# Optimization experiments

Hardware: AMD Instinct MI355X
Metric: run time of the kernel (lower is better)

Reference implementation:

```python
import jax, jax.numpy as jnp
import numpy as np

# BERT-base geometry
B, N, H, DH = 4, 512, 12, 64
HID = H * DH            # 768
E = 65536               # total edges (~avg degree 32)
NREL = 64               # relation vocabulary


def setup_inputs() -> dict:
    key = jax.random.key(0)
    ks = jax.random.split(key, 12)
    node_states = jax.random.normal(ks[0], (B, N, HID), jnp.float32)
    b = jax.random.randint(ks[1], (E,), 0, B)
    hn = jax.random.randint(ks[2], (E,), 0, N)
    tn = jax.random.randint(ks[3], (E,), 0, N)
    r = jax.random.randint(ks[4], (E,), 0, NREL)
    edge_indices = jnp.stack([b, hn, tn, r]).astype(jnp.int32)  # (4, E)
    node_type_ids = jnp.zeros((B, N), jnp.int32)  # unused by this subclass
    sc = 0.02
    Wq = jax.random.normal(ks[5], (HID, HID), jnp.float32) * sc
    bq = jnp.zeros((HID,), jnp.float32)
    Wk = jax.random.normal(ks[6], (HID, HID), jnp.float32) * sc
    bk = jnp.zeros((HID,), jnp.float32)
    Wv = jax.random.normal(ks[7], (HID, HID), jnp.float32) * sc
    bv = jnp.zeros((HID,), jnp.float32)
    # relation matrix embeddings: one (DH, DH) matrix per relation id
    rel_emb = jnp.eye(DH, dtype=jnp.float32)[None] + jax.random.normal(ks[8], (NREL, DH, DH), jnp.float32) * sc
    return {"node_states": node_states, "edge_indices": edge_indices,
            "node_type_ids": node_type_ids, "Wq": Wq, "bq": bq,
            "Wk": Wk, "bk": bk, "Wv": Wv, "bv": bv, "rel_emb": rel_emb}


def reference(node_states, edge_indices, node_type_ids, Wq, bq, Wk, bk, Wv, bv, rel_emb):
    Bq, Nn, hid = node_states.shape
    # dense QKV projections (torch Linear: y = x @ W^T + b)
    Q = node_states @ Wq.T + bq
    K = node_states @ Wk.T + bk
    V = (node_states @ Wv.T + bv).reshape(Bq, Nn, H, DH)  # (B,N,H,D)
    be, he, te, re = edge_indices  # each (E,)
    # per-edge gathers
    Qe = Q[be, he].reshape(-1, H, DH)   # (E,H,D)
    Ke = K[be, te].reshape(-1, H, DH)   # (E,H,D)
    Re = rel_emb[re]                     # (E,D,D) relation matrix per edge
    # Q projected through relation matrix, then inner product with K per head
    Qp = jnp.einsum('ehd,edk->ehk', Qe, Re)
    logits = jnp.einsum('ehd,ehd->eh', Qp, Ke) / jnp.sqrt(jnp.float32(DH))  # (E,H)
    # sparse softmax over tail nodes: segment = (batch, head_node)
    seg = be * Nn + he
    nseg = Bq * Nn
    m = jax.ops.segment_max(logits, seg, num_segments=nseg)      # (BN,H)
    ex = jnp.exp(logits - m[seg])
    denom = jax.ops.segment_sum(ex, seg, num_segments=nseg)      # (BN,H)
    p = ex / denom[seg]                                          # (E,H)
    # dropout prob = 0.0 (deterministic reference)
    # aggregate: out[b,i,h,:] = sum_edges p_e * V[b, tail_e, h, :]
    contrib = p[:, :, None] * V[be, te]                          # (E,H,D)
    out = jax.ops.segment_sum(contrib, seg, num_segments=nseg)   # (BN,H,D)
    return out.reshape(Bq, Nn, H * DH)
```

## Files before the change

kernel.cpp:

```cpp
#include <hip/hip_runtime.h>
#include <hip/hip_bf16.h>

#define NB   4
#define NN   512
#define NH   12
#define DHD  64
#define HID  768
#define NE   65536
#define NSEG 2048
#define NREL 64
#define NSUB 32
#define NRSUB (NREL * NSUB)

typedef short bf16x8 __attribute__((ext_vector_type(8)));
typedef float f32x4  __attribute__((ext_vector_type(4)));

__device__ __forceinline__ unsigned short f2bf(float f) {
    __hip_bfloat16 h = __float2bfloat16(f);
    return *reinterpret_cast<unsigned short*>(&h);
}
__device__ __forceinline__ float bf2f(unsigned short s) {
    return __int_as_float(((int)s) << 16);
}
__device__ __forceinline__ void load_lds16(const void* g, void* l) {
    __builtin_amdgcn_global_load_lds(
        (const __attribute__((address_space(1))) unsigned int*)g,
        (__attribute__((address_space(3))) unsigned int*)l, 16, 0, 0);
}

#define NX4 ((2048 * 768) / 4)
#define NW4 ((768 * 768) / 4)
__global__ __launch_bounds__(256) void cast_kernel(
    const float* __restrict__ X, const float* __restrict__ Wq,
    const float* __restrict__ Wk, const float* __restrict__ Wv,
    unsigned short* __restrict__ Xh, unsigned short* __restrict__ Wh)
{
    const int i = blockIdx.x * 256 + threadIdx.x;
    float4 v;
    ushort4* dst;
    if (i < NX4) {
        v = ((const float4*)X)[i];
        dst = &((ushort4*)Xh)[i];
    } else {
        const int j = i - NX4;
        const float* W = (j < NW4) ? Wq : ((j < 2 * NW4) ? Wk : Wv);
        const int jj = (j < NW4) ? j : ((j < 2 * NW4) ? j - NW4 : j - 2 * NW4);
        v = ((const float4*)W)[jj];
        dst = &((ushort4*)Wh)[j];
    }
    ushort4 r;
    r.x = f2bf(v.x); r.y = f2bf(v.y); r.z = f2bf(v.z); r.w = f2bf(v.w);
    *dst = r;
}

__global__ __launch_bounds__(256) void qkv_mfma(
    const unsigned short* __restrict__ Xh, const unsigned short* __restrict__ Wh,
    const float* __restrict__ bq, const float* __restrict__ bk,
    const float* __restrict__ bv,
    unsigned short* __restrict__ Qh, unsigned short* __restrict__ Kh,
    float* __restrict__ Vo)
{
    const int z = blockIdx.z;
    const unsigned short* W = Wh + (size_t)z * (768 * 768);
    const float* bias = (z == 0) ? bq : ((z == 1) ? bk : bv);

    const int n0 = blockIdx.x * 128;
    const int m0 = blockIdx.y * 128;
    const int tid  = threadIdx.x;
    const int lane = tid & 63;
    const int wave = tid >> 6;
    const int wm = wave >> 1, wn = wave & 1;

    __shared__ unsigned short As[128 * 64];
    __shared__ unsigned short Bs[128 * 64];

    f32x4 acc[4][4];
    #pragma unroll
    for (int a = 0; a < 4; ++a)
        #pragma unroll
        for (int b = 0; b < 4; ++b) acc[a][b] = (f32x4){0.f, 0.f, 0.f, 0.f};

    const int ml = lane & 15;
    const int q4 = lane >> 4;

    for (int k0 = 0; k0 < HID; k0 += 64) {
        __syncthreads();
        #pragma unroll
        for (int l = 0; l < 4; ++l) {
            const int idx = (l * 4 + wave) * 64 + lane;
            const int row = idx >> 3;
            const int kq  = (idx & 7) ^ (row & 7);
            load_lds16(Xh + (size_t)(m0 + row) * HID + k0 + kq * 8,
                       As + (l * 4 + wave) * 512);
            load_lds16(W + (size_t)(n0 + row) * HID + k0 + kq * 8,
                       Bs + (l * 4 + wave) * 512);
        }
        __syncthreads();

        #pragma unroll
        for (int ks = 0; ks < 2; ++ks) {
            bf16x8 af[4], bfr[4];
            #pragma unroll
            for (int t = 0; t < 4; ++t) {
                const int ar = wm * 64 + t * 16 + ml;
                const int ac = (ks * 4 + q4) ^ (ar & 7);
                af[t] = *(const bf16x8*)(As + ar * 64 + ac * 8);
                const int br = wn * 64 + t * 16 + ml;
                const int bc = (ks * 4 + q4) ^ (br & 7);
                bfr[t] = *(const bf16x8*)(Bs + br * 64 + bc * 8);
            }
            #pragma unroll
            for (int mt = 0; mt < 4; ++mt)
                #pragma unroll
                for (int nt = 0; nt < 4; ++nt)
                    acc[mt][nt] = __builtin_amdgcn_mfma_f32_16x16x32_bf16(
                        af[mt], bfr[nt], acc[mt][nt], 0, 0, 0);
        }
    }

    #pragma unroll
    for (int nt = 0; nt < 4; ++nt) {
        const int col = n0 + wn * 64 + nt * 16 + ml;
        const float bcol = bias[col];
        #pragma unroll
        for (int mt = 0; mt < 4; ++mt) {
            const int row = m0 + wm * 64 + mt * 16 + q4 * 4;
            #pragma unroll
            for (int rg = 0; rg < 4; ++rg) {
                const float v = acc[mt][nt][rg] + bcol;
                const size_t o = (size_t)(row + rg) * HID + col;
                if (z == 0)      Qh[o] = f2bf(v);
                else if (z == 1) Kh[o] = f2bf(v);
                else             Vo[o] = v;
            }
        }
    }
}

__global__ void hist_kernel(const int* __restrict__ ei,
                            int* __restrict__ count, int* __restrict__ rcount2)
{
    const int e = blockIdx.x * 256 + threadIdx.x;
    const int b  = ei[e];
    const int hn = ei[NE + e];
    const int rr = ei[3 * NE + e];
    const int sub = (e >> 8) & (NSUB - 1);
    atomicAdd(&count[b * NN + hn], 1);
    atomicAdd(&rcount2[rr * NSUB + sub], 1);
}

__global__ void scan_kernel(const int* __restrict__ cnt, int* __restrict__ ofs)
{
    __shared__ int buf[256];
    const int tid = threadIdx.x;
    int local[8];
    int s = 0;
    #pragma unroll
    for (int i = 0; i < 8; ++i) { local[i] = cnt[tid * 8 + i]; s += local[i]; }
    buf[tid] = s;
    __syncthreads();
    for (int off = 1; off < 256; off <<= 1) {
        const int v = (tid >= off) ? buf[tid - off] : 0;
        __syncthreads();
        buf[tid] += v;
        __syncthreads();
    }
    int run = buf[tid] - s;
    #pragma unroll
    for (int i = 0; i < 8; ++i) { ofs[tid * 8 + i] = run; run += local[i]; }
    if (tid == 255) ofs[2048] = run;
}

__global__ void scatter_kernel(const int* __restrict__ ei, const int* __restrict__ offs,
                               int* __restrict__ cursor,
                               const int* __restrict__ rofs2, int* __restrict__ rcursor2,
                               int* __restrict__ s_te, int* __restrict__ s_seg,
                               int* __restrict__ r_pos)
{
    const int e = blockIdx.x * 256 + threadIdx.x;
    const int b  = ei[e];
    const int hn = ei[NE + e];
    const int tn = ei[2 * NE + e];
    const int rr = ei[3 * NE + e];
    const int sub = (e >> 8) & (NSUB - 1);
    const int seg = b * NN + hn;
    const int pos = offs[seg] + atomicAdd(&cursor[seg], 1);
    s_te[pos]  = tn;
    s_seg[pos] = seg;
    const int rb = rr * NSUB + sub;
    const int rj = atomicAdd(&rcursor2[rb], 1);
    r_pos[rofs2[rb] + rj] = pos;
}

__global__ __launch_bounds__(256) void rel_logits(
    const unsigned short* __restrict__ Qh, const unsigned short* __restrict__ Kh,
    const float* __restrict__ rel,
    const int* __restrict__ rofs2, const int* __restrict__ r_pos,
    const int* __restrict__ s_te, const int* __restrict__ s_seg,
    float* __restrict__ Lg)
{
    const int r = blockIdx.x;
    const int rstart = rofs2[r * NSUB];
    const int rows = (rofs2[(r + 1) * NSUB] - rstart) * NH;
    const int tid = threadIdx.x;
    const int lane = tid & 63;
    const int wave = tid >> 6;

    __shared__ float ReS[64][65];
    __shared__ int qb[256], kb[256], oi[256];
    __shared__ float QpS[4][16][67];

    {
        const float* Rg = rel + (size_t)r * 4096;
        for (int i = tid; i < 1024; i += 256) {
            const float4 v = ((const float4*)Rg)[i];
            const int row = i >> 4, c4 = (i & 15) * 4;
            ReS[row][c4] = v.x; ReS[row][c4 + 1] = v.y;
            ReS[row][c4 + 2] = v.z; ReS[row][c4 + 3] = v.w;
        }
    }
    __syncthreads();

    bf16x8 bfrag[2][4];
    {
        const int q4 = lane >> 4, n = lane & 15;
        #pragma unroll
        for (int ks = 0; ks < 2; ++ks)
            #pragma unroll
            for (int nt = 0; nt < 4; ++nt) {
                bf16x8 f;
                #pragma unroll
                for (int j = 0; j < 8; ++j)
                    f[j] = (short)f2bf(ReS[ks * 32 + q4 * 8 + j][nt * 16 + n]);
                bfrag[ks][nt] = f;
            }
    }

    for (int t0 = blockIdx.y * 256; t0 < rows; t0 += gridDim.y * 256) {
        __syncthreads();
        {
            const int rowid = t0 + tid;
            if (rowid < rows) {
                const int el = rowid / 12;
                const int h  = rowid - el * 12;
                const int pos = r_pos[rstart + el];
                const int seg = s_seg[pos];
                const int te  = s_te[pos];
                const int b   = seg >> 9;
                qb[tid] = seg * HID + h * 64;
                kb[tid] = (b * NN + te) * HID + h * 64;
                oi[tid] = pos * NH + h;
            } else { qb[tid] = 0; kb[tid] = 0; oi[tid] = -1; }
        }
        __syncthreads();

        for (int g = wave; g < 16; g += 4) {
            const int m = lane & 15, q4 = lane >> 4;
            const int qbase = qb[g * 16 + m];
            f32x4 cfr[4] = {{0,0,0,0},{0,0,0,0},{0,0,0,0},{0,0,0,0}};
            #pragma unroll
            for (int ks = 0; ks < 2; ++ks) {
                const bf16x8 afr = *(const bf16x8*)(Qh + qbase + ks * 32 + q4 * 8);
                #pragma unroll
                for (int nt = 0; nt < 4; ++nt)
                    cfr[nt] = __builtin_amdgcn_mfma_f32_16x16x32_bf16(
                        afr, bfrag[ks][nt], cfr[nt], 0, 0, 0);
            }
            #pragma unroll
            for (int nt = 0; nt < 4; ++nt)
                #pragma unroll
                for (int rg = 0; rg < 4; ++rg)
                    QpS[wave][q4 * 4 + rg][nt * 16 + m] = cfr[nt][rg];
            __syncthreads();

            const int rw = lane >> 2, ch = (lane & 3) * 16;
            const int rowid2 = g * 16 + rw;
            const int kbase = kb[rowid2];
            const bf16x8 k0 = *(const bf16x8*)(Kh + kbase + ch);
            const bf16x8 k1 = *(const bf16x8*)(Kh + kbase + ch + 8);
            float s = 0.f;
            #pragma unroll
            for (int i = 0; i < 8; ++i) {
                s = fmaf(QpS[wave][rw][ch + i],     bf2f((unsigned short)k0[i]), s);
                s = fmaf(QpS[wave][rw][ch + 8 + i], bf2f((unsigned short)k1[i]), s);
            }
            s += __shfl_xor(s, 1, 64);
            s += __shfl_xor(s, 2, 64);
            if ((lane & 3) == 0) {
                const int o = oi[rowid2];
                if (o >= 0) Lg[o] = s * 0.125f;
            }
            __syncthreads();
        }
    }
}

__global__ __launch_bounds__(256) void seg_softmax_agg(
    const float* __restrict__ V, const float* __restrict__ Lg,
    const int* __restrict__ offs, const int* __restrict__ s_te,
    float* __restrict__ out)
{
    const int seg  = blockIdx.x;
    const int tid  = threadIdx.x;
    const int start = offs[seg];
    const int cnt   = offs[seg + 1] - start;
    const int browbase = seg & ~(NN - 1);

    __shared__ float lg[64 * NH];
    __shared__ int   te_s[64];
    __shared__ float mh[NH], lh[NH], ah[NH];

    if (tid < NH) { mh[tid] = -1e30f; lh[tid] = 0.f; }

    float acc0 = 0.f, acc1 = 0.f, acc2 = 0.f;
    const int hh = tid >> 6;
    const int dd = tid & 63;

    for (int c0 = 0; c0 < cnt; c0 += 64) {
        const int cc = min(64, cnt - c0);
        __syncthreads();
        if (tid < cc) te_s[tid] = s_te[start + c0 + tid];
        for (int i = tid; i < cc * NH; i += 256)
            lg[i] = Lg[(start + c0) * NH + i];
        __syncthreads();

        if (tid < NH) {
            const int h = tid;
            float mx = mh[h];
            for (int j = 0; j < cc; ++j) mx = fmaxf(mx, lg[j * NH + h]);
            const float alpha = __expf(mh[h] - mx);
            float ssum = 0.f;
            for (int j = 0; j < cc; ++j) {
                const float p = __expf(lg[j * NH + h] - mx);
                lg[j * NH + h] = p;
                ssum += p;
            }
            lh[h] = lh[h] * alpha + ssum;
            mh[h] = mx;
            ah[h] = alpha;
        }
        __syncthreads();

        const float a0 = ah[hh], a1 = ah[4 + hh], a2 = ah[8 + hh];
        acc0 *= a0; acc1 *= a1; acc2 *= a2;
        for (int j = 0; j < cc; ++j) {
            const int row = browbase + te_s[j];
            const float* __restrict__ Vr = V + (size_t)row * HID + dd;
            acc0 = fmaf(lg[j * NH + hh],     Vr[hh * 64],       acc0);
            acc1 = fmaf(lg[j * NH + 4 + hh], Vr[(4 + hh) * 64], acc1);
            acc2 = fmaf(lg[j * NH + 8 + hh], Vr[(8 + hh) * 64], acc2);
        }
    }
    __syncthreads();

    const float l0 = lh[hh], l1 = lh[4 + hh], l2 = lh[8 + hh];
    float* Yo = out + (size_t)seg * HID;
    Yo[tid]       = (l0 > 0.f) ? acc0 / l0 : 0.f;
    Yo[tid + 256] = (l1 > 0.f) ? acc1 / l1 : 0.f;
    Yo[tid + 512] = (l2 > 0.f) ? acc2 / l2 : 0.f;
}

extern "C" void kernel_launch(void* const* d_in, const int* in_sizes, int n_in,
                              void* d_out, int out_size, void* d_ws, size_t ws_size,
                              hipStream_t stream)
{
    const float* X   = (const float*)d_in[0];
    const int*   EI  = (const int*)d_in[1];
    const float* Wq  = (const float*)d_in[3];
    const float* bq  = (const float*)d_in[4];
    const float* Wk  = (const float*)d_in[5];
    const float* bk  = (const float*)d_in[6];
    const float* Wv  = (const float*)d_in[7];
    const float* bv  = (const float*)d_in[8];
    const float* rel = (const float*)d_in[9];
    float* out = (float*)d_out;

    char* p = (char*)d_ws;
    unsigned short* Qh = (unsigned short*)p;  p += (size_t)NSEG * HID * 2;
    unsigned short* Kh = (unsigned short*)p;  p += (size_t)NSEG * HID * 2;
    float* Vb = (float*)p;                    p += (size_t)NSEG * HID * 4;
    unsigned short* Xh = (unsigned short*)p;
    float* Lg = (float*)p;                    p += (size_t)NE * NH * 4;
    unsigned short* Wh = (unsigned short*)p;  p += (size_t)3 * 768 * 768 * 2;
    int* offs     = (int*)p;                  p += 2052 * 4;
    int* rofs2    = (int*)p;                  p += (NRSUB + 4) * 4;
    int* count    = (int*)p;                  p += NSEG * 4;
    int* cursor   = (int*)p;                  p += NSEG * 4;
    int* rcount2  = (int*)p;                  p += NRSUB * 4;
    int* rcursor2 = (int*)p;                  p += NRSUB * 4;
    int* s_te     = (int*)p;                  p += NE * 4;
    int* s_seg    = (int*)p;                  p += NE * 4;
    int* r_pos    = (int*)p;                  p += NE * 4;

    cast_kernel<<<(NX4 + 3 * NW4 + 255) / 256, 256, 0, stream>>>(
        X, Wq, Wk, Wv, Xh, Wh);
    qkv_mfma<<<dim3(HID / 128, (NB * NN) / 128, 3), 256, 0, stream>>>(
        Xh, Wh, bq, bk, bv, Qh, Kh, Vb);

    hipMemsetAsync(count, 0, (2 * NSEG + 2 * NRSUB) * sizeof(int), stream);
    hist_kernel<<<NE / 256, 256, 0, stream>>>(EI, count, rcount2);
    scan_kernel<<<1, 256, 0, stream>>>(count, offs);
    scan_kernel<<<1, 256, 0, stream>>>(rcount2, rofs2);
    scatter_kernel<<<NE / 256, 256, 0, stream>>>(EI, offs, cursor, rofs2, rcursor2,
                                                 s_te, s_seg, r_pos);

    rel_logits<<<dim3(NREL, 32), 256, 0, stream>>>(Qh, Kh, rel, rofs2, r_pos,
                                                   s_te, s_seg, Lg);
    seg_softmax_agg<<<NSEG, 256, 0, stream>>>(Vb, Lg, offs, s_te, out);
}
```

Before: 192.6 us.

## Parallelize segment softmax with wave shuffles and drop barriers in logit kernel

Replaces the serial per-head softmax, where 12 threads loop over each edge chunk, with per-wave online softmax. Max and sum are computed by cross-lane shuffle reductions, and probabilities are staged in per-wave LDS slots. The two block-wide barriers in the logit kernel are removed because its LDS scratch is per-wave, and the logit buffer row stride is padded from 12 to 16 floats. The aim is to cut serialization and barrier stalls, at the cost of redundant reductions per wave and a larger logit buffer.

```diff
diff --git a/kernel.cpp b/kernel.cpp
--- a/kernel.cpp
+++ b/kernel.cpp
@@ -11,6 +11,7 @@
 #define NREL 64
 #define NSUB 32
 #define NRSUB (NREL * NSUB)
+#define LGS  16
 
 typedef short bf16x8 __attribute__((ext_vector_type(8)));
 typedef float f32x4  __attribute__((ext_vector_type(4)));
@@ -249,7 +250,7 @@
                 const int b   = seg >> 9;
                 qb[tid] = seg * HID + h * 64;
                 kb[tid] = (b * NN + te) * HID + h * 64;
-                oi[tid] = pos * NH + h;
+                oi[tid] = pos * LGS + h;
             } else { qb[tid] = 0; kb[tid] = 0; oi[tid] = -1; }
         }
         __syncthreads();
@@ -271,7 +272,6 @@
                 #pragma unroll
                 for (int rg = 0; rg < 4; ++rg)
                     QpS[wave][q4 * 4 + rg][nt * 16 + m] = cfr[nt][rg];
-            __syncthreads();
 
             const int rw = lane >> 2, ch = (lane & 3) * 16;
             const int rowid2 = g * 16 + rw;
@@ -290,7 +290,6 @@
                 const int o = oi[rowid2];
                 if (o >= 0) Lg[o] = s * 0.125f;
             }
-            __syncthreads();
         }
     }
 }
@@ -302,58 +301,63 @@
 {
     const int seg  = blockIdx.x;
     const int tid  = threadIdx.x;
+    const int lane = tid & 63;
+    const int w    = tid >> 6;
     const int start = offs[seg];
     const int cnt   = offs[seg + 1] - start;
     const int browbase = seg & ~(NN - 1);
 
-    __shared__ float lg[64 * NH];
     __shared__ int   te_s[64];
-    __shared__ float mh[NH], lh[NH], ah[NH];
-
-    if (tid < NH) { mh[tid] = -1e30f; lh[tid] = 0.f; }
-
+    __shared__ float pv[4][3][64];
+
+    float m0 = -1e30f, m1 = -1e30f, m2 = -1e30f;
+    float l0 = 0.f, l1 = 0.f, l2 = 0.f;
     float acc0 = 0.f, acc1 = 0.f, acc2 = 0.f;
-    const int hh = tid >> 6;
-    const int dd = tid & 63;
 
     for (int c0 = 0; c0 < cnt; c0 += 64) {
         const int cc = min(64, cnt - c0);
         __syncthreads();
         if (tid < cc) te_s[tid] = s_te[start + c0 + tid];
-        for (int i = tid; i < cc * NH; i += 256)
-            lg[i] = Lg[(start + c0) * NH + i];
-        __syncthreads();
-
-        if (tid < NH) {
-            const int h = tid;
-            float mx = mh[h];
-            for (int j = 0; j < cc; ++j) mx = fmaxf(mx, lg[j * NH + h]);
-            const float alpha = __expf(mh[h] - mx);
-            float ssum = 0.f;
-            for (int j = 0; j < cc; ++j) {
-                const float p = __expf(lg[j * NH + h] - mx);
-                lg[j * NH + h] = p;
-                ssum += p;
-            }
-            lh[h] = lh[h] * alpha + ssum;
-            mh[h] = mx;
-            ah[h] = alpha;
-        }
-        __syncthreads();
-
-        const float a0 = ah[hh], a1 = ah[4 + hh], a2 = ah[8 + hh];
+        __syncthreads();
+
+        float g0 = -1e30f, g1 = -1e30f, g2 = -1e30f;
+        if (lane < cc) {
+            const float* Lp = Lg + (size_t)(start + c0 + lane) * LGS;
+            g0 = Lp[w]; g1 = Lp[4 + w]; g2 = Lp[8 + w];
+        }
+        float x0 = g0, x1 = g1, x2 = g2;
+        #pragma unroll
+        for (int o = 1; o < 64; o <<= 1) {
+            x0 = fmaxf(x0, __shfl_xor(x0, o, 64));
+            x1 = fmaxf(x1, __shfl_xor(x1, o, 64));
+            x2 = fmaxf(x2, __shfl_xor(x2, o, 64));
+        }
+        const float nm0 = fmaxf(m0, x0), nm1 = fmaxf(m1, x1), nm2 = fmaxf(m2, x2);
+        const float a0 = __expf(m0 - nm0), a1 = __expf(m1 - nm1), a2 = __expf(m2 - nm2);
+        float p0 = (lane < cc) ? __expf(g0 - nm0) : 0.f;
+        float p1 = (lane < cc) ? __expf(g1 - nm1) : 0.f;
+        float p2 = (lane < cc) ? __expf(g2 - nm2) : 0.f;
+        float s0 = p0, s1 = p1, s2 = p2;
+        #pragma unroll
+        for (int o = 1; o < 64; o <<= 1) {
+            s0 += __shfl_xor(s0, o, 64);
+            s1 += __shfl_xor(s1, o, 64);
+            s2 += __shfl_xor(s2, o, 64);
+        }
+        l0 = l0 * a0 + s0; l1 = l1 * a1 + s1; l2 = l2 * a2 + s2;
+        m0 = nm0; m1 = nm1; m2 = nm2;
+        pv[w][0][lane] = p0; pv[w][1][lane] = p1; pv[w][2][lane] = p2;
+
         acc0 *= a0; acc1 *= a1; acc2 *= a2;
         for (int j = 0; j < cc; ++j) {
-            const int row = browbase + te_s[j];
-            const float* __restrict__ Vr = V + (size_t)row * HID + dd;
-            acc0 = fmaf(lg[j * NH + hh],     Vr[hh * 64],       acc0);
-            acc1 = fmaf(lg[j * NH + 4 + hh], Vr[(4 + hh) * 64], acc1);
-            acc2 = fmaf(lg[j * NH + 8 + hh], Vr[(8 + hh) * 64], acc2);
-        }
-    }
-    __syncthreads();
-
-    const float l0 = lh[hh], l1 = lh[4 + hh], l2 = lh[8 + hh];
+            const float* __restrict__ Vr =
+                V + (size_t)(browbase + te_s[j]) * HID + lane;
+            acc0 = fmaf(pv[w][0][j], Vr[w * 64],       acc0);
+            acc1 = fmaf(pv[w][1][j], Vr[(4 + w) * 64], acc1);
+            acc2 = fmaf(pv[w][2][j], Vr[(8 + w) * 64], acc2);
+        }
+    }
+
     float* Yo = out + (size_t)seg * HID;
     Yo[tid]       = (l0 > 0.f) ? acc0 / l0 : 0.f;
     Yo[tid + 256] = (l1 > 0.f) ? acc1 / l1 : 0.f;
@@ -380,7 +384,7 @@
     unsigned short* Kh = (unsigned short*)p;  p += (size_t)NSEG * HID * 2;
     float* Vb = (float*)p;                    p += (size_t)NSEG * HID * 4;
     unsigned short* Xh = (unsigned short*)p;
-    float* Lg = (float*)p;                    p += (size_t)NE * NH * 4;
+    float* Lg = (float*)p;                    p += (size_t)NE * LGS * 4;
     unsigned short* Wh = (unsigned short*)p;  p += (size_t)3 * 768 * 768 * 2;
     int* offs     = (int*)p;                  p += 2052 * 4;
     int* rofs2    = (int*)p;                  p += (NRSUB + 4) * 4;
```

New measurement: 188.0 us. 1.02x faster.
